# Kernel tuning notes

Measured on AMD Instinct MI355X. Metric: run time of the kernel, lower is better.

Reference implementation:

```python
import jax, jax.numpy as jnp
import numpy as np

D_MODEL = 768
N_HEADS = 12
D_HEAD = 64
INIT_RANGE = 0.02
IGNORE = -100000.0


def setup_inputs() -> dict:
    key = jax.random.key(0)
    ks = jax.random.split(key, 5)
    x = jax.random.normal(ks[0], (2, 2048, D_MODEL), dtype=jnp.float32)
    W_Q = INIT_RANGE * jax.random.normal(ks[1], (N_HEADS, D_MODEL, D_HEAD), dtype=jnp.float32)
    W_K = INIT_RANGE * jax.random.normal(ks[2], (N_HEADS, D_MODEL, D_HEAD), dtype=jnp.float32)
    W_V = INIT_RANGE * jax.random.normal(ks[3], (N_HEADS, D_MODEL, D_HEAD), dtype=jnp.float32)
    W_O = INIT_RANGE * jax.random.normal(ks[4], (N_HEADS, D_HEAD, D_MODEL), dtype=jnp.float32)
    b_Q = jnp.zeros((N_HEADS, D_HEAD), dtype=jnp.float32)
    b_K = jnp.zeros((N_HEADS, D_HEAD), dtype=jnp.float32)
    b_V = jnp.zeros((N_HEADS, D_HEAD), dtype=jnp.float32)
    b_O = jnp.zeros((D_MODEL,), dtype=jnp.float32)
    return {"x": x, "W_Q": W_Q, "b_Q": b_Q, "W_K": W_K, "b_K": b_K,
            "W_V": W_V, "b_V": b_V, "W_O": W_O, "b_O": b_O}


def reference(x, W_Q, b_Q, W_K, b_K, W_V, b_V, W_O, b_O):
    # x: [b, s, m]; W_*: [h, m, d]
    Q = jnp.einsum('bsm,hmd->bshd', x, W_Q) + b_Q  # [b, s, h, d]
    K = jnp.einsum('bsm,hmd->bshd', x, W_K) + b_K
    V = jnp.einsum('bsm,hmd->bshd', x, W_V) + b_V
    scores = jnp.einsum('bqhd,bkhd->bhqk', Q, K) / jnp.sqrt(jnp.float32(D_HEAD))
    s = scores.shape[-1]
    causal = jnp.triu(jnp.ones((s, s), dtype=bool), k=1)  # True above diagonal
    scores = jnp.where(causal, jnp.float32(IGNORE), scores)
    pattern = jax.nn.softmax(scores, axis=-1)  # [b, h, q, k]
    Z = jnp.einsum('bhqk,bkhd->bqhd', pattern, V)
    out = jnp.einsum('bqhd,hdm->bqm', Z, W_O) + b_O
    return out
```

## Files before the change

kernel.cpp:

```cpp
#include <hip/hip_runtime.h>
#include <hip/hip_bf16.h>

#define BATCH 2
#define SLEN 2048
#define NH 12
#define DM 768
#define DH 64
#define ROWS (BATCH*SLEN)
#define NQKV (3*DM)
#define NCHUNK 40

typedef __attribute__((ext_vector_type(8))) short bf16x8;
typedef __attribute__((ext_vector_type(4))) float f32x4;
typedef unsigned short u16;
typedef unsigned int u32;
typedef __attribute__((ext_vector_type(4))) unsigned short u16x4;
typedef __attribute__((ext_vector_type(8))) unsigned short u16x8;

__device__ __forceinline__ u16 f2b(float f) {
    unsigned int u = __builtin_bit_cast(unsigned int, f);
    unsigned int r = (u + 0x7FFFu + ((u >> 16) & 1u)) >> 16;
    return (u16)r;
}
__device__ __forceinline__ float b2f(u16 v) {
    unsigned int u = ((unsigned int)v) << 16;
    return __builtin_bit_cast(float, u);
}

__device__ __forceinline__ void gload16(const u16* g, u16* l) {
    __builtin_amdgcn_global_load_lds(
        (const __attribute__((address_space(1))) unsigned int*)g,
        (__attribute__((address_space(3))) unsigned int*)l,
        16, 0, 0);
}


__global__ __launch_bounds__(256) void pack_x(const float* __restrict__ x, u16* __restrict__ xb) {
    int i = blockIdx.x * 256 + threadIdx.x;
    const float4* xv = (const float4*)x;
    float4 a = xv[i * 2], b = xv[i * 2 + 1];
    u16x8 o;
    o[0] = f2b(a.x); o[1] = f2b(a.y); o[2] = f2b(a.z); o[3] = f2b(a.w);
    o[4] = f2b(b.x); o[5] = f2b(b.y); o[6] = f2b(b.z); o[7] = f2b(b.w);
    *(u16x8*)(xb + (size_t)i * 8) = o;
}

__global__ __launch_bounds__(256) void pack_wqkv(const float* __restrict__ WQ, const float* __restrict__ WK,
                                                 const float* __restrict__ WV, u16* __restrict__ out) {
    __shared__ u16 L[64 * 72];
    int mt = blockIdx.x, h = blockIdx.y, sel = blockIdx.z;
    const float* W = sel == 0 ? WQ : (sel == 1 ? WK : WV);
    const float* src = W + ((size_t)h * DM + mt * 64) * DH;
    int t = threadIdx.x;
    for (int j = 0; j < 4; j++) {
        int i = t + 256 * j;
        int r = i >> 4, cf = i & 15;
        float4 v = ((const float4*)src)[i];
        u16x4 o; o[0] = f2b(v.x); o[1] = f2b(v.y); o[2] = f2b(v.z); o[3] = f2b(v.w);
        *(u16x4*)&L[r * 72 + cf * 4] = o;
    }
    __syncthreads();
    u16* orow = out + ((size_t)(sel * DM + h * DH)) * DM + mt * 64;
    for (int j = 0; j < 16; j++) {
        int e = t + 256 * j;
        int d = e >> 6, mm = e & 63;
        orow[(size_t)d * DM + mm] = L[mm * 72 + d];
    }
}

__global__ __launch_bounds__(256) void pack_wo(const float* __restrict__ WO, u16* __restrict__ out) {
    __shared__ u16 L[64 * 72];
    int bi = blockIdx.x, bj = blockIdx.y;
    int t = threadIdx.x;
    for (int j = 0; j < 4; j++) {
        int i = t + 256 * j;
        int r = i >> 4, cf = i & 15;
        float4 v = ((const float4*)(WO + (size_t)(bi * 64 + r) * DM + bj * 64))[cf];
        u16x4 o; o[0] = f2b(v.x); o[1] = f2b(v.y); o[2] = f2b(v.z); o[3] = f2b(v.w);
        *(u16x4*)&L[r * 72 + cf * 4] = o;
    }
    __syncthreads();
    for (int j = 0; j < 16; j++) {
        int e = t + 256 * j;
        int c = e >> 6, r = e & 63;
        out[(size_t)(bj * 64 + c) * DM + bi * 64 + r] = L[r * 72 + c];
    }
}


__global__ __launch_bounds__(256) void gemm_qkv(const u16* __restrict__ A, const u16* __restrict__ Bt,
                                                const float* __restrict__ bQ, const float* __restrict__ bK,
                                                const float* __restrict__ bV,
                                                u16* __restrict__ Qb, u16* __restrict__ Kb, u16* __restrict__ Vb) {
    __shared__ u16 Al[128 * 64];
    __shared__ u16 Bl[128 * 64];
    int t = threadIdx.x;
    int n0 = blockIdx.x * 128, m0 = blockIdx.y * 128;
    int lane = t & 63, w = t >> 6;
    int ln = lane & 15, qd = lane >> 4;
    int wr = (w & 1) * 64, wc = (w >> 1) * 64;
    int srow = lane >> 3, slot = lane & 7;
    f32x4 acc[4][4] = {};

    for (int kt = 0; kt < DM / 64; kt++) {
        __syncthreads();
        for (int j = 0; j < 4; j++) {
            int r = w * 32 + j * 8 + srow;
            int gc = slot ^ (r & 7);
            gload16(A + (size_t)(m0 + r) * DM + kt * 64 + gc * 8, &Al[(w * 32 + j * 8) * 64]);
            gload16(Bt + (size_t)(n0 + r) * DM + kt * 64 + gc * 8, &Bl[(w * 32 + j * 8) * 64]);
        }
        __syncthreads();
        for (int ks = 0; ks < 2; ks++) {
            int sl = ((ks * 4 + qd) ^ (ln & 7)) * 8;
            bf16x8 af[4], bfr[4];
            for (int rt = 0; rt < 4; rt++)
                af[rt] = *(const bf16x8*)&Al[(wr + rt * 16 + ln) * 64 + sl];
            for (int ct = 0; ct < 4; ct++)
                bfr[ct] = *(const bf16x8*)&Bl[(wc + ct * 16 + ln) * 64 + sl];
            for (int rt = 0; rt < 4; rt++)
                for (int ct = 0; ct < 4; ct++)
                    acc[rt][ct] = __builtin_amdgcn_mfma_f32_16x16x32_bf16(af[rt], bfr[ct], acc[rt][ct], 0, 0, 0);
        }
    }
    int sel = n0 / DM;
    if (sel == 2) {
        for (int ct = 0; ct < 4; ct++) {
            int col = n0 - 2 * DM + wc + ct * 16 + ln;
            int hh = col >> 6, dd = col & 63;
            float bv = bV[col];
            for (int rt = 0; rt < 4; rt++) {
                int row = m0 + wr + rt * 16 + qd * 4;
                int bb = row >> 11, ss = row & 2047;
                u16x4 pk;
                for (int r = 0; r < 4; r++) pk[r] = f2b(acc[rt][ct][r] + bv);
                *(u16x4*)&Vb[(((size_t)bb * NH + hh) * DH + dd) * SLEN + ss] = pk;
            }
        }
    } else {
        const float* bias = sel == 0 ? bQ : bK;
        u16* Out = sel == 0 ? Qb : Kb;
        const float qs = sel == 0 ? 0.125f * 1.44269504f : 1.0f;
        for (int ct = 0; ct < 4; ct++) {
            int col = n0 - sel * DM + wc + ct * 16 + ln;
            int hh = col >> 6, dd = col & 63;
            float bv = bias[col];
            for (int rt = 0; rt < 4; rt++) {
                int row = m0 + wr + rt * 16 + qd * 4;
                for (int r = 0; r < 4; r++) {
                    int rg = row + r;
                    int bb = rg >> 11, ss = rg & 2047;
                    Out[(((size_t)bb * NH + hh) * SLEN + ss) * DH + dd] = f2b((acc[rt][ct][r] + bv) * qs);
                }
            }
        }
    }
}


__device__ __forceinline__ void cid2qc(int cid, int& p, int& c, int& nc) {
    if (cid < 4)       { p = cid;                  c = 0;               nc = 1; }
    else if (cid < 12) { p = 4 + ((cid - 4) >> 1);  c = (cid - 4) & 1;   nc = 2; }
    else if (cid < 24) { p = 8 + (cid - 12) / 3;    c = (cid - 12) % 3;  nc = 3; }
    else               { p = 12 + ((cid - 24) >> 2); c = (cid - 24) & 3; nc = 4; }
}

__global__ __launch_bounds__(256, 4) void attn(const u16* __restrict__ Qb, const u16* __restrict__ Kb,
                                               const u16* __restrict__ Vtg,
                                               u16* __restrict__ Po, float* __restrict__ Plv) {
    __shared__ u16 Kl[64 * 64];
    __shared__ u16 Vt[64 * 64];
    __shared__ u16 Pq[4 * 32 * 72];
    int cid = blockIdx.x, bh = blockIdx.y;
    int p, c, nc;
    cid2qc(cid, p, c, nc);
    int ntiles = 2 * p + 2;
    int kt0 = c * ntiles / nc, kt1 = (c + 1) * ntiles / nc;
    const u16* Qp = Qb + (size_t)bh * SLEN * DH;
    const u16* Kp = Kb + (size_t)bh * SLEN * DH;
    const u16* Vp = Vtg + (size_t)bh * SLEN * DH;
    int t = threadIdx.x, lane = t & 63, w = t >> 6;
    int ln = lane & 15, qd = lane >> 4;
    int srow = lane >> 3, slot = lane & 7;
    int qbA = p * 128 + w * 32, qbB = qbA + 16;

    bf16x8 qfA[2], qfB[2];
    for (int ks = 0; ks < 2; ks++) {
        qfA[ks] = *(const bf16x8*)(Qp + (size_t)(qbA + ln) * DH + ks * 32 + qd * 8);
        qfB[ks] = *(const bf16x8*)(Qp + (size_t)(qbB + ln) * DH + ks * 32 + qd * 8);
    }

    float lA = 0.f, lB = 0.f;
    f32x4 oA[4] = {}, oB[4] = {};

    u16* PwA = Pq + w * 32 * 72;
    u16* PwB = PwA + 16 * 72;

    for (int kt = kt0; kt < kt1; kt++) {
        int k0 = kt * 64;
        __syncthreads();
        for (int j = 0; j < 2; j++) {
            int r = w * 16 + j * 8 + srow;
            int gc = slot ^ (r & 7);
            gload16(Kp + (size_t)(k0 + r) * DH + gc * 8, &Kl[(w * 16 + j * 8) * 64]);
            gload16(Vp + (size_t)r * SLEN + k0 + gc * 8, &Vt[(w * 16 + j * 8) * 64]);
        }
        __syncthreads();

        f32x4 sfA[4] = {}, sfB[4] = {};
        for (int ks = 0; ks < 2; ks++) {
            int sl = ((ks * 4 + qd) ^ (ln & 7)) * 8;
            for (int ct = 0; ct < 4; ct++) {
                bf16x8 kf = *(const bf16x8*)&Kl[(ct * 16 + ln) * 64 + sl];
                sfA[ct] = __builtin_amdgcn_mfma_f32_16x16x32_bf16(kf, qfA[ks], sfA[ct], 0, 0, 0);
                sfB[ct] = __builtin_amdgcn_mfma_f32_16x16x32_bf16(kf, qfB[ks], sfB[ct], 0, 0, 0);
            }
        }

        if (kt >= (qbA >> 6)) {
            int qg = qbA + ln;
            for (int ct = 0; ct < 4; ct++)
                for (int r = 0; r < 4; r++) {
                    int kg = k0 + ct * 16 + qd * 4 + r;
                    if (kg > qg) sfA[ct][r] = -1e30f;
                }
        }
        if (kt >= (qbB >> 6)) {
            int qg = qbB + ln;
            for (int ct = 0; ct < 4; ct++)
                for (int r = 0; r < 4; r++) {
                    int kg = k0 + ct * 16 + qd * 4 + r;
                    if (kg > qg) sfB[ct][r] = -1e30f;
                }
        }

        float sA = 0.f, sB = 0.f;
        for (int ct = 0; ct < 4; ct++) {
            u32 ea[4], eb[4];
            for (int r = 0; r < 4; r++) {
                float eA = exp2f(sfA[ct][r]);
                float eB = exp2f(sfB[ct][r]);
                ea[r] = __builtin_bit_cast(u32, eA);
                eb[r] = __builtin_bit_cast(u32, eB);
                sA += __builtin_bit_cast(float, ea[r] & 0xFFFF0000u);
                sB += __builtin_bit_cast(float, eb[r] & 0xFFFF0000u);
            }
            uint2 pkA, pkB;
            pkA.x = __builtin_amdgcn_perm(ea[1], ea[0], 0x07060302u);
            pkA.y = __builtin_amdgcn_perm(ea[3], ea[2], 0x07060302u);
            pkB.x = __builtin_amdgcn_perm(eb[1], eb[0], 0x07060302u);
            pkB.y = __builtin_amdgcn_perm(eb[3], eb[2], 0x07060302u);
            *(uint2*)&PwA[ln * 72 + ct * 16 + qd * 4] = pkA;
            *(uint2*)&PwB[ln * 72 + ct * 16 + qd * 4] = pkB;
        }
        lA += sA; lB += sB;

        for (int ks = 0; ks < 2; ks++) {
            int sl = ((ks * 4 + qd) ^ (ln & 7)) * 8;
            bf16x8 pfA = *(const bf16x8*)&PwA[ln * 72 + ks * 32 + qd * 8];
            bf16x8 pfB = *(const bf16x8*)&PwB[ln * 72 + ks * 32 + qd * 8];
            for (int dt = 0; dt < 4; dt++) {
                bf16x8 vf = *(const bf16x8*)&Vt[(dt * 16 + ln) * 64 + sl];
                oA[dt] = __builtin_amdgcn_mfma_f32_16x16x32_bf16(vf, pfA, oA[dt], 0, 0, 0);
                oB[dt] = __builtin_amdgcn_mfma_f32_16x16x32_bf16(vf, pfB, oB[dt], 0, 0, 0);
            }
        }
    }

    lA += __shfl_xor(lA, 16, 64);
    lA += __shfl_xor(lA, 32, 64);
    lB += __shfl_xor(lB, 16, 64);
    lB += __shfl_xor(lB, 32, 64);

    size_t pid = (size_t)bh * NCHUNK + cid;
    u16* op = Po + pid * 8192;
    for (int dt = 0; dt < 4; dt++) {
        u16x4 ovA, ovB;
        for (int r = 0; r < 4; r++) { ovA[r] = f2b(oA[dt][r]); ovB[r] = f2b(oB[dt][r]); }
        *(u16x4*)&op[(w * 32 + ln) * 64 + dt * 16 + qd * 4] = ovA;
        *(u16x4*)&op[(w * 32 + 16 + ln) * 64 + dt * 16 + qd * 4] = ovB;
    }
    if (qd == 0) {
        Plv[pid * 128 + w * 32 + ln] = lA;
        Plv[pid * 128 + w * 32 + 16 + ln] = lB;
    }
}


__global__ __launch_bounds__(256) void combine(const u16* __restrict__ Po, const float* __restrict__ Plv,
                                               u16* __restrict__ Zb) {
    int p = blockIdx.x, bh = blockIdx.y;
    int b = bh / NH, h = bh % NH;
    int nc, base;
    if (p < 4)       { base = p;                  nc = 1; }
    else if (p < 8)  { base = 4 + (p - 4) * 2;    nc = 2; }
    else if (p < 12) { base = 12 + (p - 8) * 3;   nc = 3; }
    else             { base = 24 + (p - 12) * 4;  nc = 4; }
    int t = threadIdx.x;
    int q = t >> 1, dseg = (t & 1) * 32;

    float acc[32] = {};
    float lsum = 0.f;
    for (int cc = 0; cc < nc; cc++) {
        size_t pid = (size_t)bh * NCHUNK + base + cc;
        lsum += Plv[pid * 128 + q];
        const u16* op = Po + pid * 8192 + q * 64 + dseg;
        for (int j = 0; j < 4; j++) {
            u16x8 v = *(const u16x8*)(op + j * 8);
            for (int e = 0; e < 8; e++)
                acc[j * 8 + e] += b2f(v[e]);
        }
    }
    float inv = 1.0f / lsum;
    u16* Zp = Zb + ((size_t)b * SLEN + p * 128 + q) * DM + h * DH + dseg;
    for (int j = 0; j < 4; j++) {
        u16x8 ov;
        for (int e = 0; e < 8; e++) ov[e] = f2b(acc[j * 8 + e] * inv);
        *(u16x8*)(Zp + j * 8) = ov;
    }
}


__global__ __launch_bounds__(256) void gemm_proj(const u16* __restrict__ A, const u16* __restrict__ Bt,
                                                 const float* __restrict__ bO, float* __restrict__ out) {
    __shared__ u16 Al[64 * 64];
    __shared__ u16 Bl[96 * 64];
    int t = threadIdx.x;
    int n0 = blockIdx.x * 96, m0 = blockIdx.y * 64;
    int lane = t & 63, w = t >> 6;
    int ln = lane & 15, qd = lane >> 4;
    int wr = (w & 1) * 32, wc = (w >> 1) * 48;
    int srow = lane >> 3, slot = lane & 7;
    f32x4 acc[2][3] = {};

    for (int kt = 0; kt < DM / 64; kt++) {
        __syncthreads();
        for (int j = 0; j < 2; j++) {
            int r = w * 16 + j * 8 + srow;
            int gc = slot ^ (r & 7);
            gload16(A + (size_t)(m0 + r) * DM + kt * 64 + gc * 8, &Al[(w * 16 + j * 8) * 64]);
        }
        for (int j = 0; j < 3; j++) {
            int r = w * 24 + j * 8 + srow;
            int gc = slot ^ (r & 7);
            gload16(Bt + (size_t)(n0 + r) * DM + kt * 64 + gc * 8, &Bl[(w * 24 + j * 8) * 64]);
        }
        __syncthreads();
        for (int ks = 0; ks < 2; ks++) {
            int sl = ((ks * 4 + qd) ^ (ln & 7)) * 8;
            bf16x8 af[2], bfr[3];
            for (int rt = 0; rt < 2; rt++)
                af[rt] = *(const bf16x8*)&Al[(wr + rt * 16 + ln) * 64 + sl];
            for (int ct = 0; ct < 3; ct++)
                bfr[ct] = *(const bf16x8*)&Bl[(wc + ct * 16 + ln) * 64 + sl];
            for (int rt = 0; rt < 2; rt++)
                for (int ct = 0; ct < 3; ct++)
                    acc[rt][ct] = __builtin_amdgcn_mfma_f32_16x16x32_bf16(af[rt], bfr[ct], acc[rt][ct], 0, 0, 0);
        }
    }
    for (int ct = 0; ct < 3; ct++) {
        int col = n0 + wc + ct * 16 + ln;
        float bv = bO[col];
        for (int rt = 0; rt < 2; rt++) {
            int row = m0 + wr + rt * 16 + qd * 4;
            for (int r = 0; r < 4; r++)
                out[(size_t)(row + r) * DM + col] = acc[rt][ct][r] + bv;
        }
    }
}


extern "C" void kernel_launch(void* const* d_in, const int* in_sizes, int n_in,
                              void* d_out, int out_size, void* d_ws, size_t ws_size,
                              hipStream_t stream) {
    const float* x  = (const float*)d_in[0];
    const float* WQ = (const float*)d_in[1];
    const float* bQ = (const float*)d_in[2];
    const float* WK = (const float*)d_in[3];
    const float* bK = (const float*)d_in[4];
    const float* WV = (const float*)d_in[5];
    const float* bV = (const float*)d_in[6];
    const float* WO = (const float*)d_in[7];
    const float* bO = (const float*)d_in[8];
    float* out = (float*)d_out;

    u16* xb   = (u16*)d_ws;
    u16* wqkv = xb + (size_t)ROWS * DM;
    u16* wo   = wqkv + (size_t)NQKV * DM;
    u16* Qb   = wo + (size_t)DM * DM;
    size_t hsz = (size_t)BATCH * NH * SLEN * DH;
    u16* Kb   = Qb + hsz;
    u16* Vb   = Kb + hsz;
    u16* Zb   = Vb + hsz;
    u16* Po   = Zb + (size_t)ROWS * DM;
    float* Pl = (float*)(Po + (size_t)BATCH * NH * NCHUNK * 8192);

    pack_x<<<ROWS * DM / 2048, 256, 0, stream>>>(x, xb);
    pack_wqkv<<<dim3(12, 12, 3), 256, 0, stream>>>(WQ, WK, WV, wqkv);
    pack_wo<<<dim3(12, 12), 256, 0, stream>>>(WO, wo);
    gemm_qkv<<<dim3(NQKV / 128, ROWS / 128), 256, 0, stream>>>(xb, wqkv, bQ, bK, bV, Qb, Kb, Vb);
    attn<<<dim3(NCHUNK, BATCH * NH), 256, 0, stream>>>(Qb, Kb, Vb, Po, Pl);
    combine<<<dim3(SLEN / 128, BATCH * NH), 256, 0, stream>>>(Po, Pl, Zb);
    gemm_proj<<<dim3(DM / 96, ROWS / 64), 256, 0, stream>>>(Zb, wo, bO, out);
}
```

Baseline: 180.7 us.

## Prefetch K/V tiles into registers and rebalance causal chunk split

Replaces the direct global-to-LDS tile loads with a register prefetch of the next K/V tile, issued after the barrier so the global load overlaps the current tile's MFMA work. Changes the causal work partition from 40 chunks to 51, with chunks per query block growing every three blocks for finer load balance. Also drops the padded P buffer stride in favour of an XOR-swizzled layout to cut LDS usage and bank conflicts. The costs are extra registers for the prefetch, a loop-based chunk lookup, and more partial outputs for the combine kernel to merge.

```diff
diff --git a/kernel.cpp b/kernel.cpp
--- a/kernel.cpp
+++ b/kernel.cpp
@@ -8,7 +8,7 @@
 #define DH 64
 #define ROWS (BATCH*SLEN)
 #define NQKV (3*DM)
-#define NCHUNK 40
+#define NCHUNK 51
 
 typedef __attribute__((ext_vector_type(8))) short bf16x8;
 typedef __attribute__((ext_vector_type(4))) float f32x4;
@@ -159,10 +159,13 @@
 
 
 __device__ __forceinline__ void cid2qc(int cid, int& p, int& c, int& nc) {
-    if (cid < 4)       { p = cid;                  c = 0;               nc = 1; }
-    else if (cid < 12) { p = 4 + ((cid - 4) >> 1);  c = (cid - 4) & 1;   nc = 2; }
-    else if (cid < 24) { p = 8 + (cid - 12) / 3;    c = (cid - 12) % 3;  nc = 3; }
-    else               { p = 12 + ((cid - 24) >> 2); c = (cid - 24) & 3; nc = 4; }
+    p = 0;
+    int base = 0;
+    while (true) {
+        int n = p / 3 + 1;
+        if (cid < base + n) { c = cid - base; nc = n; return; }
+        base += n; p++;
+    }
 }
 
 __global__ __launch_bounds__(256, 4) void attn(const u16* __restrict__ Qb, const u16* __restrict__ Kb,
@@ -170,7 +173,7 @@
                                                u16* __restrict__ Po, float* __restrict__ Plv) {
     __shared__ u16 Kl[64 * 64];
     __shared__ u16 Vt[64 * 64];
-    __shared__ u16 Pq[4 * 32 * 72];
+    __shared__ u16 Pq[4 * 32 * 64];
     int cid = blockIdx.x, bh = blockIdx.y;
     int p, c, nc;
     cid2qc(cid, p, c, nc);
@@ -193,19 +196,31 @@
     float lA = 0.f, lB = 0.f;
     f32x4 oA[4] = {}, oB[4] = {};
 
-    u16* PwA = Pq + w * 32 * 72;
-    u16* PwB = PwA + 16 * 72;
+    u16* PwA = Pq + w * 32 * 64;
+    u16* PwB = PwA + 16 * 64;
+
+    u16x8 kr[2], vr[2];
+    auto preload = [&](int kt) {
+        int k0 = kt * 64;
+        for (int j = 0; j < 2; j++) {
+            int r = w * 16 + j * 8 + srow;
+            int gc = slot ^ (srow & 7);
+            kr[j] = *(const u16x8*)(Kp + (size_t)(k0 + r) * DH + gc * 8);
+            vr[j] = *(const u16x8*)(Vp + (size_t)r * SLEN + k0 + gc * 8);
+        }
+    };
+    preload(kt0);
 
     for (int kt = kt0; kt < kt1; kt++) {
         int k0 = kt * 64;
         __syncthreads();
         for (int j = 0; j < 2; j++) {
             int r = w * 16 + j * 8 + srow;
-            int gc = slot ^ (r & 7);
-            gload16(Kp + (size_t)(k0 + r) * DH + gc * 8, &Kl[(w * 16 + j * 8) * 64]);
-            gload16(Vp + (size_t)r * SLEN + k0 + gc * 8, &Vt[(w * 16 + j * 8) * 64]);
-        }
-        __syncthreads();
+            *(u16x8*)&Kl[r * 64 + slot * 8] = kr[j];
+            *(u16x8*)&Vt[r * 64 + slot * 8] = vr[j];
+        }
+        __syncthreads();
+        if (kt + 1 < kt1) preload(kt + 1);
 
         f32x4 sfA[4] = {}, sfB[4] = {};
         for (int ks = 0; ks < 2; ks++) {
@@ -250,15 +265,16 @@
             pkA.y = __builtin_amdgcn_perm(ea[3], ea[2], 0x07060302u);
             pkB.x = __builtin_amdgcn_perm(eb[1], eb[0], 0x07060302u);
             pkB.y = __builtin_amdgcn_perm(eb[3], eb[2], 0x07060302u);
-            *(uint2*)&PwA[ln * 72 + ct * 16 + qd * 4] = pkA;
-            *(uint2*)&PwB[ln * 72 + ct * 16 + qd * 4] = pkB;
+            int off = (((ct * 2 + (qd >> 1)) ^ (ln & 7)) * 8) + (qd & 1) * 4;
+            *(uint2*)&PwA[ln * 64 + off] = pkA;
+            *(uint2*)&PwB[ln * 64 + off] = pkB;
         }
         lA += sA; lB += sB;
 
         for (int ks = 0; ks < 2; ks++) {
             int sl = ((ks * 4 + qd) ^ (ln & 7)) * 8;
-            bf16x8 pfA = *(const bf16x8*)&PwA[ln * 72 + ks * 32 + qd * 8];
-            bf16x8 pfB = *(const bf16x8*)&PwB[ln * 72 + ks * 32 + qd * 8];
+            bf16x8 pfA = *(const bf16x8*)&PwA[ln * 64 + sl];
+            bf16x8 pfB = *(const bf16x8*)&PwB[ln * 64 + sl];
             for (int dt = 0; dt < 4; dt++) {
                 bf16x8 vf = *(const bf16x8*)&Vt[(dt * 16 + ln) * 64 + sl];
                 oA[dt] = __builtin_amdgcn_mfma_f32_16x16x32_bf16(vf, pfA, oA[dt], 0, 0, 0);
@@ -291,11 +307,9 @@
                                                u16* __restrict__ Zb) {
     int p = blockIdx.x, bh = blockIdx.y;
     int b = bh / NH, h = bh % NH;
-    int nc, base;
-    if (p < 4)       { base = p;                  nc = 1; }
-    else if (p < 8)  { base = 4 + (p - 4) * 2;    nc = 2; }
-    else if (p < 12) { base = 12 + (p - 8) * 3;   nc = 3; }
-    else             { base = 24 + (p - 12) * 4;  nc = 4; }
+    int g = p / 3, i = p % 3;
+    int nc = g + 1;
+    int base = 3 * (g * (g + 1) / 2) + i * (g + 1);
     int t = threadIdx.x;
     int q = t >> 1, dseg = (t & 1) * 32;
 
```

Result: slower. 204.4 us (+13.1%).
